# Kernel optimization log

Measured on AMD Instinct MI355X. Metric: run time of the kernel, lower is better.

## Reference

```python
import jax, jax.numpy as jnp
import numpy as np

B, HH, WW, C = 1, 96, 96, 128
HEADS, K = 4, 7

def setup_inputs() -> dict:
    key = jax.random.key(0)
    ks = jax.random.split(key, 6)
    def lin(k, o, i):
        return jax.random.normal(k, (o, i), jnp.float32) * (1.0 / np.sqrt(i))
    return {
        "x": jax.random.normal(ks[0], (B, HH, WW, C), jnp.float32),
        "qkv_w": lin(ks[1], 3 * C, C),
        "qkv_b": jnp.zeros((3 * C,), jnp.float32),
        "proj_w": lin(ks[2], C, C),
        "proj_b": jnp.zeros((C,), jnp.float32),
        "fc1_w": lin(ks[3], 4 * C, C),
        "fc1_b": jnp.zeros((4 * C,), jnp.float32),
        "fc2_w": lin(ks[4], C, 4 * C),
        "fc2_b": jnp.zeros((C,), jnp.float32),
    }

def _na2d(q, k, v):
    # q,k,v: [B, heads, H, W, hd]; NATTEN 2D neighborhood attention,
    # kernel K, stride 1, dilation 1, non-causal. Windows are clamped at
    # borders so each query attends to exactly K*K in-bounds keys.
    Bq, h, Hs, Ws, hd = q.shape
    start_h = jnp.clip(jnp.arange(Hs) - K // 2, 0, Hs - K)
    idx_h = start_h[:, None] + jnp.arange(K)  # [H, K]
    start_w = jnp.clip(jnp.arange(Ws) - K // 2, 0, Ws - K)
    idx_w = start_w[:, None] + jnp.arange(K)  # [W, K]
    I = idx_h[:, None, :, None]  # -> [H, W, K, K] broadcast
    J = idx_w[None, :, None, :]
    k_nb = k[:, :, I, J, :]  # [B, heads, H, W, K, K, hd]
    v_nb = v[:, :, I, J, :]
    scale = jnp.asarray(hd, q.dtype) ** -0.5
    logits = jnp.einsum('bhijd,bhijkld->bhijkl', q, k_nb) * scale
    attn = jax.nn.softmax(logits.reshape(Bq, h, Hs, Ws, K * K), axis=-1)
    attn = attn.reshape(Bq, h, Hs, Ws, K, K)
    return jnp.einsum('bhijkl,bhijkld->bhijd', attn, v_nb)

def reference(x, qkv_w, qkv_b, proj_w, proj_b, fc1_w, fc1_b, fc2_w, fc2_b):
    Bq, Hs, Ws, Cc = x.shape
    hd = Cc // HEADS
    qkv = x @ qkv_w.T + qkv_b  # [B,H,W,3C]
    q, k, v = jnp.split(qkv, 3, axis=-1)
    def to_heads(t):
        return t.reshape(Bq, Hs, Ws, HEADS, hd).transpose(0, 3, 1, 2, 4)
    o = _na2d(to_heads(q), to_heads(k), to_heads(v))  # [B,heads,H,W,hd]
    o = o.transpose(0, 2, 3, 1, 4).reshape(Bq, Hs, Ws, Cc)
    x0 = o @ proj_w.T + proj_b
    h1 = jax.nn.gelu(x0 @ fc1_w.T + fc1_b, approximate=False)
    return h1 @ fc2_w.T + fc2_b
```

## Files before the change

### kernel.cpp

```cpp
#include <hip/hip_runtime.h>

typedef __bf16 bf16_t;
typedef __bf16 bf16x8 __attribute__((ext_vector_type(8)));
typedef __bf16 bf16x4 __attribute__((ext_vector_type(4)));
typedef float f32x4 __attribute__((ext_vector_type(4)));
typedef int   i32x4 __attribute__((ext_vector_type(4)));

#define HH 96
#define WW 96
#define CC 128
#define HD 32
#define TOK (HH * WW)
#define PLANE (TOK * CC)
#define KW 7

#define W_QKV  0
#define W_PROJ 49152
#define W_FC1  65536
#define W_FC2  131072
#define W_TOT  196608

#define PATCH 10
#define PSZ 100
#define NPAD 112
#define STR 136
#define H1S 520

__device__ __forceinline__ bf16x8 cvt8(const float* __restrict__ p) {
    const f32x4 a = *(const f32x4*)p;
    const f32x4 b = *(const f32x4*)(p + 4);
    bf16x8 r;
    r[0] = (bf16_t)a[0]; r[1] = (bf16_t)a[1]; r[2] = (bf16_t)a[2]; r[3] = (bf16_t)a[3];
    r[4] = (bf16_t)b[0]; r[5] = (bf16_t)b[1]; r[6] = (bf16_t)b[2]; r[7] = (bf16_t)b[3];
    return r;
}

template <int NT>
__device__ __forceinline__ void mmaN(const bf16_t* __restrict__ A, int lda,
                                     const bf16_t* __restrict__ W, int ldb,
                                     int K, f32x4* acc) {
    const int lane = threadIdx.x & 63;
    const bf16_t* ap = A + (lane & 15) * lda + ((lane >> 4) * 8);
    const bf16_t* bp = W + (lane & 15) * ldb + ((lane >> 4) * 8);
    for (int k0 = 0; k0 < K; k0 += 32) {
        bf16x8 a = *(const bf16x8*)(ap + k0);
#pragma unroll
        for (int t = 0; t < NT; t++) {
            bf16x8 b = *(const bf16x8*)(bp + t * 16 * ldb + k0);
            acc[t] = __builtin_amdgcn_mfma_f32_16x16x32_bf16(a, b, acc[t], 0, 0, 0);
        }
    }
}

__global__ __launch_bounds__(256) void k_cvt(const float* __restrict__ qkv_w,
                                             const float* __restrict__ proj_w,
                                             const float* __restrict__ fc1_w,
                                             const float* __restrict__ fc2_w,
                                             bf16_t* __restrict__ wb) {
    const int base = (blockIdx.x * 256 + threadIdx.x) * 4;
    const float* src;
    if (base < W_PROJ)     src = qkv_w  + base;
    else if (base < W_FC1) src = proj_w + (base - W_PROJ);
    else if (base < W_FC2) src = fc1_w  + (base - W_FC1);
    else                   src = fc2_w  + (base - W_FC2);
    const f32x4 a = *(const f32x4*)src;
    bf16x4 r;
    r[0] = (bf16_t)a[0]; r[1] = (bf16_t)a[1]; r[2] = (bf16_t)a[2]; r[3] = (bf16_t)a[3];
    *(bf16x4*)(wb + base) = r;
}

__global__ __launch_bounds__(256) void k_qkv(const float* __restrict__ x,
                                             const bf16_t* __restrict__ wb,
                                             const float* __restrict__ bias,
                                             bf16_t* __restrict__ qb,
                                             bf16_t* __restrict__ kb,
                                             bf16_t* __restrict__ vb) {
    const int wid = blockIdx.x * 4 + (threadIdx.x >> 6);
    const int m0 = (wid / 12) * 16;
    const int n0 = (wid % 12) * 32;
    const int lane = threadIdx.x & 63;
    const int g = lane >> 4, li = lane & 15;
    const float* ap = x + (m0 + li) * CC + g * 8;
    const bf16_t* bp = wb + W_QKV + (n0 + li) * CC + g * 8;
    f32x4 acc[2] = {};
    for (int k0 = 0; k0 < CC; k0 += 32) {
        bf16x8 a = cvt8(ap + k0);
#pragma unroll
        for (int t = 0; t < 2; t++) {
            bf16x8 b = *(const bf16x8*)(bp + t * 16 * CC + k0);
            acc[t] = __builtin_amdgcn_mfma_f32_16x16x32_bf16(a, b, acc[t], 0, 0, 0);
        }
    }
#pragma unroll
    for (int t = 0; t < 2; t++) {
        const int n = n0 + t * 16 + li;
        const float bb = bias[n];
        const int part = n >> 7, c = n & 127;
        bf16_t* dst = (part == 0) ? qb : (part == 1) ? kb : vb;
#pragma unroll
        for (int r = 0; r < 4; r++)
            dst[(m0 + g * 4 + r) * CC + c] = (bf16_t)(acc[t][r] + bb);
    }
}

__global__ __launch_bounds__(256, 4) void k_attn(
        const bf16_t* __restrict__ qb, const bf16_t* __restrict__ kg,
        const bf16_t* __restrict__ vg, const bf16_t* __restrict__ wb,
        const float* __restrict__ proj_b, bf16_t* __restrict__ x0g) {
    __shared__ __align__(16) bf16_t Pbuf[4 * 16 * STR];
    __shared__ __align__(16) bf16_t o_s[16 * STR];
    __shared__ __align__(16) int voff[128];

    const int tid = threadIdx.x;
    const int w = tid >> 6, lane = tid & 63;
    const int g = lane >> 4, li = lane & 15;
    const int bid = blockIdx.x;
    const int i0 = (bid / 24) * 4, j0 = (bid % 24) * 4;
    const int pr0 = min(max(i0 - 3, 0), HH - PATCH);
    const int pc0 = min(max(j0 - 3, 0), WW - PATCH);
    const int head = w;
    const int ch = head * HD;

    if (tid < 128) {
        const int p = min(tid, PSZ - 1);
        const int pi = p / 10, pj = p - 10 * pi;
        voff[tid] = ((pr0 + pi) * WW + pc0 + pj) * CC;
    }
    __syncthreads();

    f32x4 lg[7];
    {
        const int qi = i0 + (li >> 2), qj = j0 + (li & 3);
        const bf16x8 aq = *(const bf16x8*)(qb + (qi * WW + qj) * CC + ch + g * 8);
#pragma unroll
        for (int t = 0; t < 7; t++) {
            const bf16x8 bk = *(const bf16x8*)(kg + voff[t * 16 + li] + ch + g * 8);
            lg[t] = __builtin_amdgcn_mfma_f32_16x16x32_bf16(aq, bk, (f32x4){0.f,0.f,0.f,0.f}, 0, 0, 0);
        }
    }
    int lr[4], lc[4];
#pragma unroll
    for (int r = 0; r < 4; r++) {
        const int m = g * 4 + r;
        const int i = i0 + (m >> 2), j = j0 + (m & 3);
        lr[r] = min(max(i - 3, 0), HH - KW) - pr0;
        lc[r] = min(max(j - 3, 0), WW - KW) - pc0;
    }
    const float scale = 0.17677669529663687f;
#pragma unroll
    for (int t = 0; t < 7; t++) {
        const int col = t * 16 + li;
        const int pi = col / 10, pj = col - 10 * pi;
#pragma unroll
        for (int r = 0; r < 4; r++) {
            const bool valid = (col < PSZ) &&
                               ((unsigned)(pi - lr[r]) <= 6u) &&
                               ((unsigned)(pj - lc[r]) <= 6u);
            lg[t][r] = valid ? lg[t][r] * scale : -1e30f;
        }
    }
    f32x4 mx = lg[0], sm;
#pragma unroll
    for (int t = 1; t < 7; t++)
#pragma unroll
        for (int r = 0; r < 4; r++) mx[r] = fmaxf(mx[r], lg[t][r]);
#pragma unroll
    for (int off = 8; off; off >>= 1)
#pragma unroll
        for (int r = 0; r < 4; r++) mx[r] = fmaxf(mx[r], __shfl_xor(mx[r], off));
#pragma unroll
    for (int r = 0; r < 4; r++) sm[r] = 0.f;
#pragma unroll
    for (int t = 0; t < 7; t++)
#pragma unroll
        for (int r = 0; r < 4; r++) {
            lg[t][r] = __expf(lg[t][r] - mx[r]);
            sm[r] += lg[t][r];
        }
#pragma unroll
    for (int off = 8; off; off >>= 1)
#pragma unroll
        for (int r = 0; r < 4; r++) sm[r] += __shfl_xor(sm[r], off);
#pragma unroll
    for (int r = 0; r < 4; r++) sm[r] = 1.f / sm[r];

    bf16_t* Pw = Pbuf + w * 16 * STR;
#pragma unroll
    for (int t = 0; t < 7; t++)
#pragma unroll
        for (int r = 0; r < 4; r++)
            Pw[(g * 4 + r) * STR + t * 16 + li] = (bf16_t)(lg[t][r] * sm[r]);
    *(bf16x4*)(Pw + (lane >> 2) * STR + NPAD + (lane & 3) * 4) = (bf16x4){0,0,0,0};
    __syncthreads();

    f32x4 oA[2] = {};
#pragma unroll
    for (int ks0 = 0; ks0 < 128; ks0 += 32) {
        const bf16x8 a = *(const bf16x8*)(Pw + li * STR + ks0 + g * 8);
        const i32x4 o0 = *(const i32x4*)&voff[ks0 + g * 8];
        const i32x4 o1 = *(const i32x4*)&voff[ks0 + g * 8 + 4];
#pragma unroll
        for (int t2 = 0; t2 < 2; t2++) {
            const int cb = ch + t2 * 16 + li;
            bf16x8 b;
            b[0] = vg[o0[0] + cb]; b[1] = vg[o0[1] + cb];
            b[2] = vg[o0[2] + cb]; b[3] = vg[o0[3] + cb];
            b[4] = vg[o1[0] + cb]; b[5] = vg[o1[1] + cb];
            b[6] = vg[o1[2] + cb]; b[7] = vg[o1[3] + cb];
            oA[t2] = __builtin_amdgcn_mfma_f32_16x16x32_bf16(a, b, oA[t2], 0, 0, 0);
        }
    }
#pragma unroll
    for (int t2 = 0; t2 < 2; t2++)
#pragma unroll
        for (int r = 0; r < 4; r++)
            o_s[(g * 4 + r) * STR + ch + t2 * 16 + li] = (bf16_t)oA[t2][r];
    __syncthreads();

    {
        f32x4 acc[2] = {};
        mmaN<2>(o_s, STR, wb + W_PROJ + (w * 32) * CC, CC, CC, acc);
#pragma unroll
        for (int t = 0; t < 2; t++) {
            const int n = w * 32 + t * 16 + li;
            const float bb = proj_b[n];
#pragma unroll
            for (int r = 0; r < 4; r++) {
                const int m = g * 4 + r;
                const int i = i0 + (m >> 2), j = j0 + (m & 3);
                x0g[(i * WW + j) * CC + n] = (bf16_t)(acc[t][r] + bb);
            }
        }
    }
}

__global__ __launch_bounds__(512, 4) void k_mlp(const bf16_t* __restrict__ x0g,
                                                const bf16_t* __restrict__ wb,
                                                const float* __restrict__ fc1_b,
                                                const float* __restrict__ fc2_b,
                                                float* __restrict__ out) {
    __shared__ __align__(16) bf16_t h1s[16 * H1S];
    const int w = threadIdx.x >> 6, lane = threadIdx.x & 63;
    const int g = lane >> 4, li = lane & 15;
    const int m0 = blockIdx.x * 16;

    {
        f32x4 acc[4] = {};
        mmaN<4>(x0g + m0 * CC, CC, wb + W_FC1 + (w * 64) * CC, CC, CC, acc);
#pragma unroll
        for (int t = 0; t < 4; t++) {
            const int n = w * 64 + t * 16 + li;
            const float bb = fc1_b[n];
#pragma unroll
            for (int r = 0; r < 4; r++) {
                const int m = g * 4 + r;
                const float xv = acc[t][r] + bb;
                const float u = 0.7978845608028654f * (xv + 0.044715f * xv * xv * xv);
                const float e = __expf(2.f * u);
                const float gg = 0.5f * xv * (2.f - 2.f / (e + 1.f));
                h1s[m * H1S + n] = (bf16_t)gg;
            }
        }
    }
    __syncthreads();
    {
        f32x4 acc[1] = {};
        mmaN<1>(h1s, H1S, wb + W_FC2 + (w * 16) * (4 * CC), 4 * CC, 4 * CC, acc);
        const int n = w * 16 + li;
        const float bb = fc2_b[n];
#pragma unroll
        for (int r = 0; r < 4; r++) {
            const int m = g * 4 + r;
            float xv = acc[0][r] + bb;
            xv = fminf(fmaxf(xv, -1e4f), 1e4f);
            out[(m0 + m) * CC + n] = xv;
        }
    }
}

extern "C" void kernel_launch(void* const* d_in, const int* in_sizes, int n_in,
                              void* d_out, int out_size, void* d_ws, size_t ws_size,
                              hipStream_t stream) {
    const float* x      = (const float*)d_in[0];
    const float* qkv_w  = (const float*)d_in[1];
    const float* qkv_b  = (const float*)d_in[2];
    const float* proj_w = (const float*)d_in[3];
    const float* proj_b = (const float*)d_in[4];
    const float* fc1_w  = (const float*)d_in[5];
    const float* fc1_b  = (const float*)d_in[6];
    const float* fc2_w  = (const float*)d_in[7];
    const float* fc2_b  = (const float*)d_in[8];

    bf16_t* ws = (bf16_t*)d_ws;
    bf16_t* qb = ws;
    bf16_t* kb = ws + PLANE;
    bf16_t* vb = ws + 2 * PLANE;
    bf16_t* x0 = ws + 3 * PLANE;
    bf16_t* wb = ws + 4 * PLANE;
    float* out = (float*)d_out;

    k_cvt <<<192,  256, 0, stream>>>(qkv_w, proj_w, fc1_w, fc2_w, wb);
    k_qkv <<<1728, 256, 0, stream>>>(x, wb, qkv_b, qb, kb, vb);
    k_attn<<<576,  256, 0, stream>>>(qb, kb, vb, wb, proj_b, x0);
    k_mlp <<<576,  512, 0, stream>>>(x0, wb, fc1_b, fc2_b, out);
}
```

Baseline: 126.6 us.

## Fuse attention with MLP and fold weight conversion into QKV kernel

Merges the attention+projection kernel with the MLP kernel so the x0 tile stays in shared memory instead of round-tripping through global memory, and reuses the probability buffer for the GELU hidden activations. The standalone weight-conversion kernel is folded into the QKV kernel, which now reads qkv weights directly in fp32 and converts on the fly, with each wave computing 64 output columns. This cuts two launches and a global intermediate, at the cost of more shared memory and registers per block (launch bounds lowered to 3 blocks per CU). The fused MLP now runs with 4 waves per 16 tokens instead of 8, which may reduce parallelism. A __syncthreads before the P·V step was also removed; this appears safe because each wave reads only its own P rows.

```diff
diff --git a/kernel.cpp b/kernel.cpp
--- a/kernel.cpp
+++ b/kernel.cpp
@@ -14,17 +14,22 @@
 #define PLANE (TOK * CC)
 #define KW 7
 
-#define W_QKV  0
-#define W_PROJ 49152
-#define W_FC1  65536
-#define W_FC2  131072
-#define W_TOT  196608
+#define W_PROJ 0
+#define W_FC1  16384
+#define W_FC2  81920
+#define W_TOT  147456
 
 #define PATCH 10
 #define PSZ 100
 #define NPAD 112
 #define STR 136
 #define H1S 520
+
+#define L_P    0
+#define L_OS   8704
+#define L_X0   10880
+#define L_VOFF 13056
+#define L_TOT  13312
 
 __device__ __forceinline__ bf16x8 cvt8(const float* __restrict__ p) {
     const f32x4 a = *(const f32x4*)p;
@@ -52,49 +57,52 @@
     }
 }
 
-__global__ __launch_bounds__(256) void k_cvt(const float* __restrict__ qkv_w,
+__global__ __launch_bounds__(256) void k_qkv(const float* __restrict__ x,
+                                             const float* __restrict__ qkv_w,
+                                             const float* __restrict__ qkv_b,
                                              const float* __restrict__ proj_w,
                                              const float* __restrict__ fc1_w,
                                              const float* __restrict__ fc2_w,
-                                             bf16_t* __restrict__ wb) {
-    const int base = (blockIdx.x * 256 + threadIdx.x) * 4;
-    const float* src;
-    if (base < W_PROJ)     src = qkv_w  + base;
-    else if (base < W_FC1) src = proj_w + (base - W_PROJ);
-    else if (base < W_FC2) src = fc1_w  + (base - W_FC1);
-    else                   src = fc2_w  + (base - W_FC2);
-    const f32x4 a = *(const f32x4*)src;
-    bf16x4 r;
-    r[0] = (bf16_t)a[0]; r[1] = (bf16_t)a[1]; r[2] = (bf16_t)a[2]; r[3] = (bf16_t)a[3];
-    *(bf16x4*)(wb + base) = r;
-}
-
-__global__ __launch_bounds__(256) void k_qkv(const float* __restrict__ x,
-                                             const bf16_t* __restrict__ wb,
-                                             const float* __restrict__ bias,
+                                             bf16_t* __restrict__ wb,
                                              bf16_t* __restrict__ qb,
                                              bf16_t* __restrict__ kb,
                                              bf16_t* __restrict__ vb) {
-    const int wid = blockIdx.x * 4 + (threadIdx.x >> 6);
-    const int m0 = (wid / 12) * 16;
-    const int n0 = (wid % 12) * 32;
-    const int lane = threadIdx.x & 63;
+    const int tid = threadIdx.x, bid = blockIdx.x;
+    {
+        const int idx = bid * 256 + tid;
+        if (idx < W_TOT / 4) {
+            const int base = idx * 4;
+            const float* src;
+            if (base < W_FC1)      src = proj_w + base;
+            else if (base < W_FC2) src = fc1_w + (base - W_FC1);
+            else                   src = fc2_w + (base - W_FC2);
+            const f32x4 a = *(const f32x4*)src;
+            bf16x4 r;
+            r[0] = (bf16_t)a[0]; r[1] = (bf16_t)a[1];
+            r[2] = (bf16_t)a[2]; r[3] = (bf16_t)a[3];
+            *(bf16x4*)(wb + base) = r;
+        }
+    }
+    const int wid = bid * 4 + (tid >> 6);
+    const int m0 = (wid / 6) * 16;
+    const int n0 = (wid % 6) * 64;
+    const int lane = tid & 63;
     const int g = lane >> 4, li = lane & 15;
     const float* ap = x + (m0 + li) * CC + g * 8;
-    const bf16_t* bp = wb + W_QKV + (n0 + li) * CC + g * 8;
-    f32x4 acc[2] = {};
+    const float* bp = qkv_w + (n0 + li) * CC + g * 8;
+    f32x4 acc[4] = {};
     for (int k0 = 0; k0 < CC; k0 += 32) {
         bf16x8 a = cvt8(ap + k0);
 #pragma unroll
-        for (int t = 0; t < 2; t++) {
-            bf16x8 b = *(const bf16x8*)(bp + t * 16 * CC + k0);
+        for (int t = 0; t < 4; t++) {
+            bf16x8 b = cvt8(bp + t * 16 * CC + k0);
             acc[t] = __builtin_amdgcn_mfma_f32_16x16x32_bf16(a, b, acc[t], 0, 0, 0);
         }
     }
 #pragma unroll
-    for (int t = 0; t < 2; t++) {
+    for (int t = 0; t < 4; t++) {
         const int n = n0 + t * 16 + li;
-        const float bb = bias[n];
+        const float bb = qkv_b[n];
         const int part = n >> 7, c = n & 127;
         bf16_t* dst = (part == 0) ? qb : (part == 1) ? kb : vb;
 #pragma unroll
@@ -103,13 +111,17 @@
     }
 }
 
-__global__ __launch_bounds__(256, 4) void k_attn(
+__global__ __launch_bounds__(256, 3) void k_attn_mlp(
         const bf16_t* __restrict__ qb, const bf16_t* __restrict__ kg,
         const bf16_t* __restrict__ vg, const bf16_t* __restrict__ wb,
-        const float* __restrict__ proj_b, bf16_t* __restrict__ x0g) {
-    __shared__ __align__(16) bf16_t Pbuf[4 * 16 * STR];
-    __shared__ __align__(16) bf16_t o_s[16 * STR];
-    __shared__ __align__(16) int voff[128];
+        const float* __restrict__ proj_b, const float* __restrict__ fc1_b,
+        const float* __restrict__ fc2_b,  float* __restrict__ out) {
+    __shared__ __align__(16) bf16_t smem[L_TOT];
+    bf16_t* Pbuf = smem + L_P;
+    bf16_t* o_s  = smem + L_OS;
+    bf16_t* x0s  = smem + L_X0;
+    bf16_t* h1s  = smem + L_P;
+    int*    voff = (int*)(smem + L_VOFF);
 
     const int tid = threadIdx.x;
     const int w = tid >> 6, lane = tid & 63;
@@ -118,8 +130,7 @@
     const int i0 = (bid / 24) * 4, j0 = (bid % 24) * 4;
     const int pr0 = min(max(i0 - 3, 0), HH - PATCH);
     const int pc0 = min(max(j0 - 3, 0), WW - PATCH);
-    const int head = w;
-    const int ch = head * HD;
+    const int ch = w * HD;
 
     if (tid < 128) {
         const int p = min(tid, PSZ - 1);
@@ -191,7 +202,6 @@
         for (int r = 0; r < 4; r++)
             Pw[(g * 4 + r) * STR + t * 16 + li] = (bf16_t)(lg[t][r] * sm[r]);
     *(bf16x4*)(Pw + (lane >> 2) * STR + NPAD + (lane & 3) * 4) = (bf16x4){0,0,0,0};
-    __syncthreads();
 
     f32x4 oA[2] = {};
 #pragma unroll
@@ -225,31 +235,18 @@
             const int n = w * 32 + t * 16 + li;
             const float bb = proj_b[n];
 #pragma unroll
-            for (int r = 0; r < 4; r++) {
-                const int m = g * 4 + r;
-                const int i = i0 + (m >> 2), j = j0 + (m & 3);
-                x0g[(i * WW + j) * CC + n] = (bf16_t)(acc[t][r] + bb);
-            }
-        }
-    }
-}
-
-__global__ __launch_bounds__(512, 4) void k_mlp(const bf16_t* __restrict__ x0g,
-                                                const bf16_t* __restrict__ wb,
-                                                const float* __restrict__ fc1_b,
-                                                const float* __restrict__ fc2_b,
-                                                float* __restrict__ out) {
-    __shared__ __align__(16) bf16_t h1s[16 * H1S];
-    const int w = threadIdx.x >> 6, lane = threadIdx.x & 63;
-    const int g = lane >> 4, li = lane & 15;
-    const int m0 = blockIdx.x * 16;
-
-    {
-        f32x4 acc[4] = {};
-        mmaN<4>(x0g + m0 * CC, CC, wb + W_FC1 + (w * 64) * CC, CC, CC, acc);
-#pragma unroll
-        for (int t = 0; t < 4; t++) {
-            const int n = w * 64 + t * 16 + li;
+            for (int r = 0; r < 4; r++)
+                x0s[(g * 4 + r) * STR + n] = (bf16_t)(acc[t][r] + bb);
+        }
+    }
+    __syncthreads();
+
+    {
+        f32x4 acc[8] = {};
+        mmaN<8>(x0s, STR, wb + W_FC1 + (w * 128) * CC, CC, CC, acc);
+#pragma unroll
+        for (int t = 0; t < 8; t++) {
+            const int n = w * 128 + t * 16 + li;
             const float bb = fc1_b[n];
 #pragma unroll
             for (int r = 0; r < 4; r++) {
@@ -263,17 +260,22 @@
         }
     }
     __syncthreads();
-    {
-        f32x4 acc[1] = {};
-        mmaN<1>(h1s, H1S, wb + W_FC2 + (w * 16) * (4 * CC), 4 * CC, 4 * CC, acc);
-        const int n = w * 16 + li;
-        const float bb = fc2_b[n];
-#pragma unroll
-        for (int r = 0; r < 4; r++) {
-            const int m = g * 4 + r;
-            float xv = acc[0][r] + bb;
-            xv = fminf(fmaxf(xv, -1e4f), 1e4f);
-            out[(m0 + m) * CC + n] = xv;
+
+    {
+        f32x4 acc[2] = {};
+        mmaN<2>(h1s, H1S, wb + W_FC2 + (w * 32) * (4 * CC), 4 * CC, 4 * CC, acc);
+#pragma unroll
+        for (int t = 0; t < 2; t++) {
+            const int n = w * 32 + t * 16 + li;
+            const float bb = fc2_b[n];
+#pragma unroll
+            for (int r = 0; r < 4; r++) {
+                const int m = g * 4 + r;
+                const int i = i0 + (m >> 2), j = j0 + (m & 3);
+                float xv = acc[t][r] + bb;
+                xv = fminf(fmaxf(xv, -1e4f), 1e4f);
+                out[(i * WW + j) * CC + n] = xv;
+            }
         }
     }
 }
@@ -292,15 +294,14 @@
     const float* fc2_b  = (const float*)d_in[8];
 
     bf16_t* ws = (bf16_t*)d_ws;
-    bf16_t* qb = ws;
-    bf16_t* kb = ws + PLANE;
-    bf16_t* vb = ws + 2 * PLANE;
-    bf16_t* x0 = ws + 3 * PLANE;
-    bf16_t* wb = ws + 4 * PLANE;
+    bf16_t* wb = ws;
+    bf16_t* qb = ws + W_TOT;
+    bf16_t* kb = qb + PLANE;
+    bf16_t* vb = kb + PLANE;
     float* out = (float*)d_out;
 
-    k_cvt <<<192,  256, 0, stream>>>(qkv_w, proj_w, fc1_w, fc2_w, wb);
-    k_qkv <<<1728, 256, 0, stream>>>(x, wb, qkv_b, qb, kb, vb);
-    k_attn<<<576,  256, 0, stream>>>(qb, kb, vb, wb, proj_b, x0);
-    k_mlp <<<576,  512, 0, stream>>>(x0, wb, fc1_b, fc2_b, out);
-}
+    k_qkv     <<<864, 256, 0, stream>>>(x, qkv_w, qkv_b, proj_w, fc1_w, fc2_w,
+                                        wb, qb, kb, vb);
+    k_attn_mlp<<<576, 256, 0, stream>>>(qb, kb, vb, wb,
+                                        proj_b, fc1_b, fc2_b, out);
+}
```

Result: faster. 122.4 us (-3.3%).
